# Kernel optimization log

Measured on AMD Instinct MI355X. Metric: run time of the kernel, lower is better.

## Reference

```python
import jax, jax.numpy as jnp
import numpy as np

NEG = -10000.0
START_TAG = 62
STOP_TAG = 63


def setup_inputs() -> dict:
    key = jax.random.key(0)
    k1, k2, k3 = jax.random.split(key, 3)
    S, B, T = 512, 512, 64
    feats = jax.random.normal(k1, (S, B, T), dtype=jnp.float32)
    tags = jax.random.randint(k2, (S, B), 0, START_TAG, dtype=jnp.int32)
    mask = jnp.ones((S, B), dtype=jnp.float32)
    # nn.Parameter(torch.randn(T,T)) with start row / stop col clamped to -1e4
    transitions = jax.random.normal(k3, (T, T), dtype=jnp.float32)
    transitions = transitions.at[START_TAG, :].set(NEG).at[:, STOP_TAG].set(NEG)
    return {"feats": feats, "tags": tags, "mask": mask, "transitions": transitions}


def _score_sentence(feats, tags, mask, transitions):
    # feats: [S,B,T], tags/mask: [S,B]
    S, B, T = feats.shape
    emission = jnp.take_along_axis(feats, tags[:, :, None], axis=2)[..., 0]  # [S,B]
    start = jnp.full((1, B), START_TAG, dtype=tags.dtype)
    tags_ext = jnp.concatenate([start, tags], axis=0)  # [S+1,B]
    trans = transitions[tags_ext[:-1], tags_ext[1:]]  # [S,B]
    score = jnp.sum((emission + trans) * mask, axis=0)  # [B]
    last_idx = mask.sum(axis=0).astype(jnp.int32) - 1  # [B]
    last_tags = tags[last_idx, jnp.arange(B)]
    return score + transitions[last_tags, STOP_TAG]


def _forward_alg(feats, mask, transitions):
    S, B, T = feats.shape
    log_alpha0 = jnp.full((B, T), NEG, dtype=feats.dtype).at[:, START_TAG].set(0.0)

    def step(log_alpha, xs):
        f_i, m_i = xs  # [B,T], [B]
        # broadcast: [B, prev_tag, next_tag]
        scores = log_alpha[:, :, None] + transitions[None, :, :] + f_i[:, None, :]
        nxt = jax.nn.logsumexp(scores, axis=1)  # [B,T]
        log_alpha = jnp.where(m_i[:, None] > 0, nxt, log_alpha)
        return log_alpha, None

    log_alpha, _ = jax.lax.scan(step, log_alpha0, (feats, mask))
    return jax.nn.logsumexp(log_alpha + transitions[STOP_TAG][None, :], axis=1)  # [B]


def reference(feats, tags, mask, transitions):
    score_true = _score_sentence(feats, tags, mask, transitions)
    log_z = _forward_alg(feats, mask, transitions)
    return jnp.mean(log_z - score_true)
```

## Files before the change

### kernel.cpp

```cpp
#include <hip/hip_runtime.h>

#define NEG (-10000.0f)
#define START_TAG 62
#define STOP_TAG 63
#define SLEN 512
#define BATCH 512
#define NTAG 64

__global__ __launch_bounds__(64) __attribute__((amdgpu_waves_per_eu(1, 1)))
void crf_fwd(const float* __restrict__ feats,
             const int* __restrict__ tags,
             const float* __restrict__ mask,
             const float* __restrict__ trans,
             float* __restrict__ diff ) {
    const int b = blockIdx.x;
    const int j = threadIdx.x;

    float e[NTAG];
    float colsum = 0.0f;
#pragma unroll
    for (int i = 0; i < NTAG; ++i) {
        e[i] = __expf(trans[i * NTAG + j]);
        colsum += e[i];
    }
    const float tstop = trans[STOP_TAG * NTAG + j];

    float mreg[8];
#pragma unroll
    for (int k = 0; k < 8; ++k)
        mreg[k] = mask[(64 * k + j) * BATCH + b];

    float f_s0 = feats[(0 * BATCH + b) * NTAG + j];
    float m0 = __uint_as_float(__builtin_amdgcn_readlane(__float_as_uint(mreg[0]), 0));
    float alpha = (m0 > 0.0f) ? (NEG + log1pf(colsum) + f_s0)
                              : ((j == START_TAG) ? 0.0f : NEG);

    const float* fp = feats + (size_t)b * NTAG + j;
    float f0 = fp[(size_t)1 * BATCH * NTAG];
    float f1 = fp[(size_t)2 * BATCH * NTAG];

#pragma unroll
    for (int k = 0; k < 8; ++k) {
        const float mcur = mreg[k];
        const int s_begin = (k == 0) ? 1 : 64 * k;
        const int s_end = 64 * k + 64;
        for (int s = s_begin; s < s_end; ++s) {
            const float fc = f0;
            f0 = f1;
            int sp = s + 2;
            if (sp > SLEN - 1) sp = SLEN - 1;
            f1 = fp[(size_t)sp * BATCH * NTAG];

            float mk = __uint_as_float(
                __builtin_amdgcn_readlane(__float_as_uint(mcur), s & 63));

            float C = __uint_as_float(
                __builtin_amdgcn_readfirstlane(__float_as_uint(alpha)));
            float p = __expf(alpha - C);

            unsigned pu = __float_as_uint(p);
            float a0 = 0.0f, a1 = 0.0f, a2 = 0.0f, a3 = 0.0f;
#pragma unroll
            for (int i = 0; i < NTAG; i += 4) {
                a0 = fmaf(__uint_as_float(__builtin_amdgcn_readlane(pu, i + 0)), e[i + 0], a0);
                a1 = fmaf(__uint_as_float(__builtin_amdgcn_readlane(pu, i + 1)), e[i + 1], a1);
                a2 = fmaf(__uint_as_float(__builtin_amdgcn_readlane(pu, i + 2)), e[i + 2], a2);
                a3 = fmaf(__uint_as_float(__builtin_amdgcn_readlane(pu, i + 3)), e[i + 3], a3);
            }
            float acc = (a0 + a1) + (a2 + a3);

            float nxt = C + __logf(acc) + fc;
            alpha = (mk > 0.0f) ? nxt : alpha;
        }
    }

    float v = alpha + tstop;
    float m2 = v;
#pragma unroll
    for (int w = 32; w >= 1; w >>= 1)
        m2 = fmaxf(m2, __shfl_xor(m2, w, 64));
    float pe = __expf(v - m2);
#pragma unroll
    for (int w = 32; w >= 1; w >>= 1)
        pe += __shfl_xor(pe, w, 64);
    float logz = m2 + __logf(pe);

    float psc = 0.0f, pms = 0.0f;
#pragma unroll
    for (int k = 0; k < 8; ++k) {
        int s = j + 64 * k;
        int tg = tags[s * BATCH + b];
        float mk = mreg[k];
        int tprev = (s == 0) ? START_TAG : tags[(s - 1) * BATCH + b];
        float em = feats[((size_t)s * BATCH + b) * NTAG + tg];
        psc = fmaf(em + trans[tprev * NTAG + tg], mk, psc);
        pms += mk;
    }
#pragma unroll
    for (int w = 32; w >= 1; w >>= 1) {
        psc += __shfl_xor(psc, w, 64);
        pms += __shfl_xor(pms, w, 64);
    }

    if (j == 0) {
        int last_idx = (int)(pms + 0.5f) - 1;
        int ltag = tags[last_idx * BATCH + b];
        float score = psc + trans[ltag * NTAG + STOP_TAG];
        diff[b] = logz - score;
    }
}

__global__ __launch_bounds__(512) void crf_reduce(const float* __restrict__ diff,
                                                  float* __restrict__ out) {
    __shared__ float sdata[8];
    int t = threadIdx.x;
    float val = diff[t];
#pragma unroll
    for (int w = 32; w >= 1; w >>= 1)
        val += __shfl_xor(val, w, 64);
    if ((t & 63) == 0) sdata[t >> 6] = val;
    __syncthreads();
    if (t == 0) {
        float ssum = 0.0f;
        for (int i = 0; i < 8; ++i) ssum += sdata[i];
        out[0] = ssum * (1.0f / (float)BATCH);
    }
}

extern "C" void kernel_launch(void* const* d_in, const int* in_sizes, int n_in,
                              void* d_out, int out_size, void* d_ws, size_t ws_size,
                              hipStream_t stream) {
    const float* feats = (const float*)d_in[0];
    const int* tags = (const int*)d_in[1];
    const float* mask = (const float*)d_in[2];
    const float* trans = (const float*)d_in[3];
    float* out = (float*)d_out;
    float* diff = (float*)d_ws;

    crf_fwd<<<BATCH, 64, 0, stream>>>(feats, tags, mask, trans, diff);
    crf_reduce<<<1, 512, 0, stream>>>(diff, out);
}
```

Baseline: 242.2 us.

## Run CRF forward recursion in linear-probability space with periodic rescaling

Replaces the per-step log-space update (readfirstlane max, exp, log) with a scaled linear-domain recursion: alpha is kept as exp-scaled probabilities, multiplied by exp(feat), and renormalized by lane 0's value only every fourth step, with the log of the scale accumulated separately. This takes a transcendental exp and log off the serial dependency chain for most steps, and exp of the emissions is computed ahead through a deeper prefetch queue. It risks underflow or overflow between renormalizations and depends on lane 0 staying a nonzero pivot, since lane 0 is used as the scale.

```diff
diff --git a/kernel.cpp b/kernel.cpp
--- a/kernel.cpp
+++ b/kernel.cpp
@@ -23,7 +23,7 @@
         e[i] = __expf(trans[i * NTAG + j]);
         colsum += e[i];
     }
-    const float tstop = trans[STOP_TAG * NTAG + j];
+    const float et_stop = __expf(trans[STOP_TAG * NTAG + j]);
 
     float mreg[8];
 #pragma unroll
@@ -35,9 +35,19 @@
     float alpha = (m0 > 0.0f) ? (NEG + log1pf(colsum) + f_s0)
                               : ((j == START_TAG) ? 0.0f : NEG);
 
+    float M = alpha;
+#pragma unroll
+    for (int w = 32; w >= 1; w >>= 1)
+        M = fmaxf(M, __shfl_xor(M, w, 64));
+    float a = __expf(alpha - M);
+    float logscale = M;
+
     const float* fp = feats + (size_t)b * NTAG + j;
-    float f0 = fp[(size_t)1 * BATCH * NTAG];
-    float f1 = fp[(size_t)2 * BATCH * NTAG];
+    const size_t STRIDE = (size_t)BATCH * NTAG;
+    float g_cur = __expf(fp[1 * STRIDE]);
+    float q0 = fp[2 * STRIDE];
+    float q1 = fp[3 * STRIDE];
+    float q2 = fp[4 * STRIDE];
 
 #pragma unroll
     for (int k = 0; k < 8; ++k) {
@@ -45,45 +55,55 @@
         const int s_begin = (k == 0) ? 1 : 64 * k;
         const int s_end = 64 * k + 64;
         for (int s = s_begin; s < s_end; ++s) {
-            const float fc = f0;
-            f0 = f1;
-            int sp = s + 2;
-            if (sp > SLEN - 1) sp = SLEN - 1;
-            f1 = fp[(size_t)sp * BATCH * NTAG];
-
             float mk = __uint_as_float(
                 __builtin_amdgcn_readlane(__float_as_uint(mcur), s & 63));
 
-            float C = __uint_as_float(
-                __builtin_amdgcn_readfirstlane(__float_as_uint(alpha)));
-            float p = __expf(alpha - C);
-
-            unsigned pu = __float_as_uint(p);
+            unsigned au = __float_as_uint(a);
             float a0 = 0.0f, a1 = 0.0f, a2 = 0.0f, a3 = 0.0f;
 #pragma unroll
-            for (int i = 0; i < NTAG; i += 4) {
-                a0 = fmaf(__uint_as_float(__builtin_amdgcn_readlane(pu, i + 0)), e[i + 0], a0);
-                a1 = fmaf(__uint_as_float(__builtin_amdgcn_readlane(pu, i + 1)), e[i + 1], a1);
-                a2 = fmaf(__uint_as_float(__builtin_amdgcn_readlane(pu, i + 2)), e[i + 2], a2);
-                a3 = fmaf(__uint_as_float(__builtin_amdgcn_readlane(pu, i + 3)), e[i + 3], a3);
+            for (int gq = 0; gq < 8; ++gq) {
+                unsigned t0 = __builtin_amdgcn_readlane(au, 8 * gq + 0);
+                unsigned t1 = __builtin_amdgcn_readlane(au, 8 * gq + 1);
+                unsigned t2 = __builtin_amdgcn_readlane(au, 8 * gq + 2);
+                unsigned t3 = __builtin_amdgcn_readlane(au, 8 * gq + 3);
+                unsigned t4 = __builtin_amdgcn_readlane(au, 8 * gq + 4);
+                unsigned t5 = __builtin_amdgcn_readlane(au, 8 * gq + 5);
+                unsigned t6 = __builtin_amdgcn_readlane(au, 8 * gq + 6);
+                unsigned t7 = __builtin_amdgcn_readlane(au, 8 * gq + 7);
+                a0 = fmaf(__uint_as_float(t0), e[8 * gq + 0], a0);
+                a1 = fmaf(__uint_as_float(t1), e[8 * gq + 1], a1);
+                a2 = fmaf(__uint_as_float(t2), e[8 * gq + 2], a2);
+                a3 = fmaf(__uint_as_float(t3), e[8 * gq + 3], a3);
+                a0 = fmaf(__uint_as_float(t4), e[8 * gq + 4], a0);
+                a1 = fmaf(__uint_as_float(t5), e[8 * gq + 5], a1);
+                a2 = fmaf(__uint_as_float(t6), e[8 * gq + 6], a2);
+                a3 = fmaf(__uint_as_float(t7), e[8 * gq + 7], a3);
             }
             float acc = (a0 + a1) + (a2 + a3);
+            float anew = acc * g_cur;
+            a = (mk > 0.0f) ? anew : a;
 
-            float nxt = C + __logf(acc) + fc;
-            alpha = (mk > 0.0f) ? nxt : alpha;
+            if ((s & 3) == 0) {
+                float C = __uint_as_float(
+                    __builtin_amdgcn_readfirstlane(__float_as_uint(a)));
+                logscale += __logf(C);
+                a *= (1.0f / C);
+            }
+
+            g_cur = __expf(q0);
+            q0 = q1;
+            q1 = q2;
+            int sp = s + 5;
+            if (sp > SLEN - 1) sp = SLEN - 1;
+            q2 = fp[(size_t)sp * STRIDE];
         }
     }
 
-    float v = alpha + tstop;
-    float m2 = v;
+    float term = a * et_stop;
 #pragma unroll
     for (int w = 32; w >= 1; w >>= 1)
-        m2 = fmaxf(m2, __shfl_xor(m2, w, 64));
-    float pe = __expf(v - m2);
-#pragma unroll
-    for (int w = 32; w >= 1; w >>= 1)
-        pe += __shfl_xor(pe, w, 64);
-    float logz = m2 + __logf(pe);
+        term += __shfl_xor(term, w, 64);
+    float logz = logscale + __logf(term);
 
     float psc = 0.0f, pms = 0.0f;
 #pragma unroll
```

Result: slower. 339.2 us (+40.0%).
